# Optimization experiments

Measured on AMD Instinct MI355X. Metric: run time of the kernel, lower is better.

## Reference

```python
import jax, jax.numpy as jnp
import numpy as np

LEAK = 0.95
EPS = 1e-4
THRESH = 1.0


def spike_fn(x):
    # forward of SurrogateBPFunction: heaviside(x > 0)
    return (x > 0).astype(x.dtype)


def setup_inputs() -> dict:
    key = jax.random.key(0)
    k1, k2, k3 = jax.random.split(key, 3)
    T, B, D_in, H, C = 20, 512, 4096, 1024, 100
    z = jax.random.normal(k1, (T, B, D_in), dtype=jnp.float32)
    # xavier_uniform with gain=2: bound = 2 * sqrt(6/(fan_in+fan_out))
    b1 = 2.0 * np.sqrt(6.0 / (D_in + H))
    W1 = jax.random.uniform(k2, (H, D_in), dtype=jnp.float32, minval=-b1, maxval=b1)
    b2 = 2.0 * np.sqrt(6.0 / (H + C))
    W2 = jax.random.uniform(k3, (C, H), dtype=jnp.float32, minval=-b2, maxval=b2)
    bn_gamma = jnp.ones((T, H), dtype=jnp.float32)
    return {"z": z, "W1": W1, "bn_gamma": bn_gamma, "W2": W2}


def reference(z, W1, bn_gamma, W2):
    T = z.shape[0]
    B = z.shape[1]
    H = W1.shape[0]
    C = W2.shape[0]

    def step(carry, xs):
        mem1, mem2 = carry
        inp_t, gamma = xs  # inp_t: [B, D_in], gamma: [H]
        h = jnp.einsum('bd,hd->bh', inp_t, W1)  # fc1, no bias
        # BatchNorm1d (training-mode batch stats, affine weight, no bias)
        mean = h.mean(axis=0)
        var = h.var(axis=0)  # biased variance, matches torch BN
        h = gamma * (h - mean) * jax.lax.rsqrt(var + EPS)
        mem1 = LEAK * mem1 + h
        mem_thr = mem1 / THRESH - 1.0
        out = spike_fn(mem_thr)
        rst = jnp.where(mem_thr > 0, THRESH, 0.0).astype(mem1.dtype)
        mem1 = mem1 - rst
        mem2 = mem2 + jnp.einsum('bh,ch->bc', out, W2)
        return (mem1, mem2), None

    mem1_0 = jnp.zeros((B, H), dtype=z.dtype)
    mem2_0 = jnp.zeros((B, C), dtype=z.dtype)
    (mem1, mem2), _ = jax.lax.scan(step, (mem1_0, mem2_0), (z, bn_gamma))
    return mem2 / T
```

## Files before the change

### kernel.cpp

```cpp
#include <hip/hip_runtime.h>
#include <hip/hip_bf16.h>
#include <stdint.h>

typedef _Float16 half8 __attribute__((ext_vector_type(8)));
typedef float f32x4 __attribute__((ext_vector_type(4)));
typedef float f32x16 __attribute__((ext_vector_type(16)));

#define T_STEPS 20
#define B_SZ 512
#define D_IN 4096
#define H_SZ 1024
#define C_SZ 100
#define M_TOT (T_STEPS * B_SZ)
#define BK 32
#define KITERS (D_IN / BK)

__device__ __forceinline__ void gload16(const _Float16* g, _Float16* l) {
  __builtin_amdgcn_global_load_lds(
      (const __attribute__((address_space(1))) void*)g,
      (__attribute__((address_space(3))) void*)l, 16, 0, 0);
}

struct HL {
  half8 h;
  half8 l;
};
__device__ __forceinline__ HL split8(float4 a, float4 b) {
  HL r;
  auto p0 = __builtin_amdgcn_cvt_pkrtz(a.x, a.y);
  auto p1 = __builtin_amdgcn_cvt_pkrtz(a.z, a.w);
  auto p2 = __builtin_amdgcn_cvt_pkrtz(b.x, b.y);
  auto p3 = __builtin_amdgcn_cvt_pkrtz(b.z, b.w);
  r.h[0] = p0.x; r.h[1] = p0.y; r.h[2] = p1.x; r.h[3] = p1.y;
  r.h[4] = p2.x; r.h[5] = p2.y; r.h[6] = p3.x; r.h[7] = p3.y;
  auto q0 = __builtin_amdgcn_cvt_pkrtz(a.x - (float)p0.x, a.y - (float)p0.y);
  auto q1 = __builtin_amdgcn_cvt_pkrtz(a.z - (float)p1.x, a.w - (float)p1.y);
  auto q2 = __builtin_amdgcn_cvt_pkrtz(b.x - (float)p2.x, b.y - (float)p2.y);
  auto q3 = __builtin_amdgcn_cvt_pkrtz(b.z - (float)p3.x, b.w - (float)p3.y);
  r.l[0] = q0.x; r.l[1] = q0.y; r.l[2] = q1.x; r.l[3] = q1.y;
  r.l[4] = q2.x; r.l[5] = q2.y; r.l[6] = q3.x; r.l[7] = q3.y;
  return r;
}

__global__ __launch_bounds__(256) void k_prep_frag(
    const float* __restrict__ Z, _Float16* __restrict__ Azh,
    _Float16* __restrict__ Azl, const float* __restrict__ W1,
    _Float16* __restrict__ Wfh, _Float16* __restrict__ Wfl) {
  __shared__ float sL[32 * 256];

  const int cc = blockIdx.x;
  int rt = blockIdx.y >> 2;
  const int rb = blockIdx.y & 3;
  const float* src;
  _Float16 *dh, *dl;
  if (rt < 80) {
    src = Z; dh = Azh; dl = Azl;
  } else {
    rt -= 80; src = W1; dh = Wfh; dl = Wfl;
  }
  const int tid = threadIdx.x;
  const int lane64 = tid & 63;
  const int w4 = tid >> 6;

  const int row_base = rt * 128 + rb * 32;
  float4 v[8];
#pragma unroll
  for (int it = 0; it < 8; ++it) {
    const int row_local = it * 4 + w4;
    v[it] = *(const float4*)(src + (int64_t)(row_base + row_local) * D_IN +
                             cc * 256 + lane64 * 4);
  }
#pragma unroll
  for (int it = 0; it < 8; ++it) {
    const int row_local = it * 4 + w4;
    const int c = (lane64 * 4) ^ ((row_local & 7) << 2);
    *(float4*)&sL[row_local * 256 + c] = v[it];
  }
  __syncthreads();

  const int s = (tid >> 6) & 1;
  const int hi = (tid >> 5) & 1;
  const int l31 = tid & 31;
  const int q = s * 2 + hi;
  const int sw = (l31 & 7) << 2;
#pragma unroll
  for (int it2 = 0; it2 < 4; ++it2) {
    const int kil = it2 * 2 + (tid >> 7);
    const int c0 = kil * 32 + q * 8;
    float4 a = *(const float4*)&sL[l31 * 256 + (c0 ^ sw)];
    float4 b = *(const float4*)&sL[l31 * 256 + ((c0 + 4) ^ sw)];
    HL hl = split8(a, b);
    const int64_t d = ((int64_t)(rt * 128 + cc * 8 + kil)) * 4096 +
                      (rb * 128 + s * 64 + hi * 32 + l31) * 8;
    *(half8*)&dh[d] = hl.h;
    *(half8*)&dl[d] = hl.l;
  }
}

__global__ void k_prep_w2(const float* __restrict__ w2, _Float16* __restrict__ hi,
                          _Float16* __restrict__ lo) {
  int i = blockIdx.x * 256 + threadIdx.x;
  float v = (i < C_SZ * H_SZ) ? w2[i] : 0.0f;
  _Float16 h = (_Float16)v;
  hi[i] = h;
  lo[i] = (_Float16)(v - (float)h);
}

__global__ __launch_bounds__(256) void k_gemm1(
    const _Float16* __restrict__ Ahi, const _Float16* __restrict__ Alo,
    const _Float16* __restrict__ Whi, const _Float16* __restrict__ Wlo,
    float* __restrict__ Hbuf) {
  __shared__ _Float16 sAh[4096];
  __shared__ _Float16 sAl[4096];
  __shared__ _Float16 sWh[4096];
  __shared__ _Float16 sWl[4096];

  const int tid = threadIdx.x;
  const int lane = tid & 63;
  const int w = tid >> 6;

  const int bid = blockIdx.x;
  const int xcd = bid & 7;
  const int qb = bid >> 3;
  const int mt = xcd * 10 + (qb >> 3);
  const int nt = qb & 7;

  const int ls = w * 512 + lane * 8;
  const _Float16* gAh = Ahi + (int64_t)mt * (128 * 4096) + ls;
  const _Float16* gAl = Alo + (int64_t)mt * (128 * 4096) + ls;
  const _Float16* gWh = Whi + (int64_t)nt * (128 * 4096) + ls;
  const _Float16* gWl = Wlo + (int64_t)nt * (128 * 4096) + ls;

  const int wm = (w >> 1) * 64;
  const int wn = (w & 1) * 64;
  const int ra = (wm >> 4) * 512 + lane * 8;
  const int rbb = (wn >> 4) * 512 + lane * 8;

  f32x16 acc[2][2] = {};

  for (int ki = 0; ki < KITERS; ++ki) {
    const int64_t so = (int64_t)ki * 4096;
    __syncthreads();
    gload16(gAh + so, &sAh[ls]);
    gload16(gAh + so + 2048, &sAh[ls + 2048]);
    gload16(gAl + so, &sAl[ls]);
    gload16(gAl + so + 2048, &sAl[ls + 2048]);
    gload16(gWh + so, &sWh[ls]);
    gload16(gWh + so + 2048, &sWh[ls + 2048]);
    gload16(gWl + so, &sWl[ls]);
    gload16(gWl + so + 2048, &sWl[ls + 2048]);
    __syncthreads();

    half8 ah[2][2], al[2][2], bh[2][2], bl[2][2];
#pragma unroll
    for (int i = 0; i < 2; ++i) {
#pragma unroll
      for (int s = 0; s < 2; ++s) {
        ah[i][s] = *(const half8*)&sAh[ra + (i * 2 + s) * 512];
        al[i][s] = *(const half8*)&sAl[ra + (i * 2 + s) * 512];
        bh[i][s] = *(const half8*)&sWh[rbb + (i * 2 + s) * 512];
        bl[i][s] = *(const half8*)&sWl[rbb + (i * 2 + s) * 512];
      }
    }
#pragma unroll
    for (int a = 0; a < 2; ++a) {
#pragma unroll
      for (int b = 0; b < 2; ++b) {
#pragma unroll
        for (int s = 0; s < 2; ++s) {
          acc[a][b] = __builtin_amdgcn_mfma_f32_32x32x16_f16(ah[a][s], bh[b][s], acc[a][b], 0, 0, 0);
          acc[a][b] = __builtin_amdgcn_mfma_f32_32x32x16_f16(ah[a][s], bl[b][s], acc[a][b], 0, 0, 0);
          acc[a][b] = __builtin_amdgcn_mfma_f32_32x32x16_f16(al[a][s], bh[b][s], acc[a][b], 0, 0, 0);
        }
      }
    }
  }

  const int64_t m0 = (int64_t)mt * 128;
  const int n0 = nt * 128;
  const int l31 = lane & 31;
  const int h2 = lane >> 5;
#pragma unroll
  for (int a = 0; a < 2; ++a) {
#pragma unroll
    for (int b = 0; b < 2; ++b) {
      float* dst = Hbuf + (m0 + wm + a * 32 + h2 * 4) * H_SZ + n0 + wn + b * 32 + l31;
#pragma unroll
      for (int r4 = 0; r4 < 4; ++r4) {
#pragma unroll
        for (int r = 0; r < 4; ++r) {
          dst[(int64_t)(r4 * 8 + r) * H_SZ] = acc[a][b][r4 * 4 + r];
        }
      }
    }
  }
}

__global__ void k_stats(const float* __restrict__ Hbuf, const float* __restrict__ gamma,
                        float* __restrict__ scale, float* __restrict__ shift) {
  const int t = blockIdx.y;
  const int tx = threadIdx.x & 63;
  const int ty = threadIdx.x >> 6;
  const int h = blockIdx.x * 64 + tx;
  const float* p = Hbuf + ((int64_t)t * B_SZ + ty * 128) * H_SZ + h;
  float s = 0.f, s2 = 0.f;
#pragma unroll 8
  for (int i = 0; i < 128; ++i) {
    float v = p[(int64_t)i * H_SZ];
    s += v;
    s2 += v * v;
  }
  __shared__ float ss[4][64];
  __shared__ float sq[4][64];
  ss[ty][tx] = s;
  sq[ty][tx] = s2;
  __syncthreads();
  if (ty == 0) {
    float a = ss[0][tx] + ss[1][tx] + ss[2][tx] + ss[3][tx];
    float b = sq[0][tx] + sq[1][tx] + sq[2][tx] + sq[3][tx];
    const float mean = a * (1.0f / B_SZ);
    const float var = b * (1.0f / B_SZ) - mean * mean;
    const float rs = rsqrtf(var + 1e-4f);
    const float sc = gamma[t * H_SZ + h] * rs;
    scale[t * H_SZ + h] = sc;
    shift[t * H_SZ + h] = -mean * sc;
  }
}

__global__ void k_recur(const float* __restrict__ Hbuf, const float* __restrict__ scale,
                        const float* __restrict__ shift, _Float16* __restrict__ S) {
  const int idx = blockIdx.x * 256 + threadIdx.x;
  const int b = idx >> 10;
  const int h = idx & 1023;
  float mem = 0.f;
  int cnt = 0;
#pragma unroll
  for (int t = 0; t < T_STEPS; ++t) {
    float v = Hbuf[((int64_t)(t * B_SZ + b) << 10) + h];
    v = v * scale[(t << 10) + h] + shift[(t << 10) + h];
    mem = 0.95f * mem + v;
    if (mem - 1.0f > 0.0f) {
      ++cnt;
      mem -= 1.0f;
    }
  }
  S[idx] = (_Float16)cnt;
}

__global__ void k_gemm2(const _Float16* __restrict__ S, const _Float16* __restrict__ W2h,
                        const _Float16* __restrict__ W2l, float* __restrict__ out) {
  const int wid = threadIdx.x >> 6;
  const int lane = threadIdx.x & 63;
  const int m0 = blockIdx.y * 64 + wid * 16;
  const int n0 = blockIdx.x * 16;
  const int fr = lane & 15;
  const int quad = lane >> 4;

  const _Float16* sp = S + (int64_t)(m0 + fr) * H_SZ + quad * 8;
  const _Float16* wph = W2h + (int64_t)(n0 + fr) * H_SZ + quad * 8;
  const _Float16* wpl = W2l + (int64_t)(n0 + fr) * H_SZ + quad * 8;

  f32x4 acc = {0.f, 0.f, 0.f, 0.f};
#pragma unroll 4
  for (int k = 0; k < H_SZ; k += 32) {
    half8 a = *(const half8*)(sp + k);
    half8 bh = *(const half8*)(wph + k);
    half8 bl = *(const half8*)(wpl + k);
    acc = __builtin_amdgcn_mfma_f32_16x16x32_f16(a, bh, acc, 0, 0, 0);
    acc = __builtin_amdgcn_mfma_f32_16x16x32_f16(a, bl, acc, 0, 0, 0);
  }
  const int col = n0 + fr;
  if (col < C_SZ) {
#pragma unroll
    for (int r = 0; r < 4; ++r) {
      const int row = m0 + quad * 4 + r;
      out[row * C_SZ + col] = acc[r] * (1.0f / T_STEPS);
    }
  }
}

extern "C" void kernel_launch(void* const* d_in, const int* in_sizes, int n_in,
                              void* d_out, int out_size, void* d_ws, size_t ws_size,
                              hipStream_t stream) {
  const float* z = (const float*)d_in[0];
  const float* W1 = (const float*)d_in[1];
  const float* gamma = (const float*)d_in[2];
  const float* W2 = (const float*)d_in[3];
  float* out = (float*)d_out;

  char* ws = (char*)d_ws;
  size_t off = 0;
  auto alloc = [&](size_t bytes) -> void* {
    void* p = ws + off;
    off += (bytes + 255) & ~(size_t)255;
    return p;
  };
  _Float16* Azh = (_Float16*)alloc((size_t)M_TOT * D_IN * 2);
  _Float16* Azl = (_Float16*)alloc((size_t)M_TOT * D_IN * 2);
  _Float16* Wfh = (_Float16*)alloc((size_t)H_SZ * D_IN * 2);
  _Float16* Wfl = (_Float16*)alloc((size_t)H_SZ * D_IN * 2);
  float* Hbuf = (float*)alloc((size_t)M_TOT * H_SZ * 4);
  float* scale = (float*)alloc((size_t)T_STEPS * H_SZ * 4);
  float* shift = (float*)alloc((size_t)T_STEPS * H_SZ * 4);
  _Float16* S = (_Float16*)alloc((size_t)B_SZ * H_SZ * 2);
  _Float16* W2h = (_Float16*)alloc((size_t)112 * H_SZ * 2);
  _Float16* W2l = (_Float16*)alloc((size_t)112 * H_SZ * 2);

  dim3 gp(16, 352);
  k_prep_frag<<<gp, 256, 0, stream>>>(z, Azh, Azl, W1, Wfh, Wfl);
  k_prep_w2<<<(112 * H_SZ) / 256, 256, 0, stream>>>(W2, W2h, W2l);

  k_gemm1<<<640, 256, 0, stream>>>(Azh, Azl, Wfh, Wfl, Hbuf);

  dim3 gs(H_SZ / 64, T_STEPS);
  k_stats<<<gs, 256, 0, stream>>>(Hbuf, gamma, scale, shift);

  k_recur<<<(B_SZ * H_SZ) / 256, 256, 0, stream>>>(Hbuf, scale, shift, S);

  dim3 g2(7, 8);
  k_gemm2<<<g2, 256, 0, stream>>>(S, W2h, W2l, out);
}
```

Baseline: 556.2 us.

## Double-buffer LDS tiles in fc1 GEMM to overlap loads with MFMA

Splits each shared-memory operand buffer into two stages and restructures the K loop so the next tile's global-to-LDS loads are issued before computing on the current tile. This is meant to hide global load latency behind MFMA work and drop one barrier per iteration. It doubles LDS usage per block, which may lower occupancy.

```diff
diff --git a/kernel.cpp b/kernel.cpp
--- a/kernel.cpp
+++ b/kernel.cpp
@@ -110,10 +110,10 @@
     const _Float16* __restrict__ Ahi, const _Float16* __restrict__ Alo,
     const _Float16* __restrict__ Whi, const _Float16* __restrict__ Wlo,
     float* __restrict__ Hbuf) {
-  __shared__ _Float16 sAh[4096];
-  __shared__ _Float16 sAl[4096];
-  __shared__ _Float16 sWh[4096];
-  __shared__ _Float16 sWl[4096];
+  __shared__ _Float16 sAh[2][4096];
+  __shared__ _Float16 sAl[2][4096];
+  __shared__ _Float16 sWh[2][4096];
+  __shared__ _Float16 sWl[2][4096];
 
   const int tid = threadIdx.x;
   const int lane = tid & 63;
@@ -138,28 +138,28 @@
 
   f32x16 acc[2][2] = {};
 
-  for (int ki = 0; ki < KITERS; ++ki) {
+  auto stage = [&](int buf, int ki) {
     const int64_t so = (int64_t)ki * 4096;
-    __syncthreads();
-    gload16(gAh + so, &sAh[ls]);
-    gload16(gAh + so + 2048, &sAh[ls + 2048]);
-    gload16(gAl + so, &sAl[ls]);
-    gload16(gAl + so + 2048, &sAl[ls + 2048]);
-    gload16(gWh + so, &sWh[ls]);
-    gload16(gWh + so + 2048, &sWh[ls + 2048]);
-    gload16(gWl + so, &sWl[ls]);
-    gload16(gWl + so + 2048, &sWl[ls + 2048]);
-    __syncthreads();
-
+    gload16(gAh + so, &sAh[buf][ls]);
+    gload16(gAh + so + 2048, &sAh[buf][ls + 2048]);
+    gload16(gAl + so, &sAl[buf][ls]);
+    gload16(gAl + so + 2048, &sAl[buf][ls + 2048]);
+    gload16(gWh + so, &sWh[buf][ls]);
+    gload16(gWh + so + 2048, &sWh[buf][ls + 2048]);
+    gload16(gWl + so, &sWl[buf][ls]);
+    gload16(gWl + so + 2048, &sWl[buf][ls + 2048]);
+  };
+
+  auto compute = [&](int buf) {
     half8 ah[2][2], al[2][2], bh[2][2], bl[2][2];
 #pragma unroll
     for (int i = 0; i < 2; ++i) {
 #pragma unroll
       for (int s = 0; s < 2; ++s) {
-        ah[i][s] = *(const half8*)&sAh[ra + (i * 2 + s) * 512];
-        al[i][s] = *(const half8*)&sAl[ra + (i * 2 + s) * 512];
-        bh[i][s] = *(const half8*)&sWh[rbb + (i * 2 + s) * 512];
-        bl[i][s] = *(const half8*)&sWl[rbb + (i * 2 + s) * 512];
+        ah[i][s] = *(const half8*)&sAh[buf][ra + (i * 2 + s) * 512];
+        al[i][s] = *(const half8*)&sAl[buf][ra + (i * 2 + s) * 512];
+        bh[i][s] = *(const half8*)&sWh[buf][rbb + (i * 2 + s) * 512];
+        bl[i][s] = *(const half8*)&sWl[buf][rbb + (i * 2 + s) * 512];
       }
     }
 #pragma unroll
@@ -174,6 +174,18 @@
         }
       }
     }
+  };
+
+  stage(0, 0);
+  __syncthreads();
+
+  for (int ki = 0; ki < KITERS; ki += 2) {
+    if (ki + 1 < KITERS) stage(1, ki + 1);
+    compute(0);
+    __syncthreads();
+    if (ki + 2 < KITERS) stage(0, ki + 2);
+    compute(1);
+    __syncthreads();
   }
 
   const int64_t m0 = (int64_t)mt * 128;
```

Measured after the change: 706.3 us. +27.0%, slower.

## Split gemm1 K dimension in two with partial planes summed downstream

Applied to the files above, without the earlier changes.

Splits the first GEMM's K loop into two halves, doubling the block count, and writes each half's result to a separate partial-sum plane. The stats and recurrence kernels read both planes and add them. This is meant to improve CU utilization and wave balance for the large GEMM. In exchange it doubles the workspace and the global traffic for the hidden activations.

```diff
diff --git a/kernel.cpp b/kernel.cpp
--- a/kernel.cpp
+++ b/kernel.cpp
@@ -14,6 +14,8 @@
 #define M_TOT (T_STEPS * B_SZ)
 #define BK 32
 #define KITERS (D_IN / BK)
+#define KHALF (KITERS / 2)
+#define HPLANE ((int64_t)M_TOT * H_SZ)
 
 __device__ __forceinline__ void gload16(const _Float16* g, _Float16* l) {
   __builtin_amdgcn_global_load_lds(
@@ -109,7 +111,7 @@
 __global__ __launch_bounds__(256) void k_gemm1(
     const _Float16* __restrict__ Ahi, const _Float16* __restrict__ Alo,
     const _Float16* __restrict__ Whi, const _Float16* __restrict__ Wlo,
-    float* __restrict__ Hbuf) {
+    float* __restrict__ Hpart) {
   __shared__ _Float16 sAh[4096];
   __shared__ _Float16 sAl[4096];
   __shared__ _Float16 sWh[4096];
@@ -121,9 +123,12 @@
 
   const int bid = blockIdx.x;
   const int xcd = bid & 7;
-  const int qb = bid >> 3;
-  const int mt = xcd * 10 + (qb >> 3);
-  const int nt = qb & 7;
+  const int q = bid >> 3;
+  const int mtl = q >> 4;
+  const int r = q & 15;
+  const int nt = r >> 1;
+  const int kh = r & 1;
+  const int mt = xcd * 10 + mtl;
 
   const int ls = w * 512 + lane * 8;
   const _Float16* gAh = Ahi + (int64_t)mt * (128 * 4096) + ls;
@@ -138,7 +143,8 @@
 
   f32x16 acc[2][2] = {};
 
-  for (int ki = 0; ki < KITERS; ++ki) {
+  const int k0 = kh * KHALF;
+  for (int ki = k0; ki < k0 + KHALF; ++ki) {
     const int64_t so = (int64_t)ki * 4096;
     __syncthreads();
     gload16(gAh + so, &sAh[ls]);
@@ -176,6 +182,7 @@
     }
   }
 
+  float* Hb = Hpart + (int64_t)kh * HPLANE;
   const int64_t m0 = (int64_t)mt * 128;
   const int n0 = nt * 128;
   const int l31 = lane & 31;
@@ -184,29 +191,30 @@
   for (int a = 0; a < 2; ++a) {
 #pragma unroll
     for (int b = 0; b < 2; ++b) {
-      float* dst = Hbuf + (m0 + wm + a * 32 + h2 * 4) * H_SZ + n0 + wn + b * 32 + l31;
+      float* dst = Hb + (m0 + wm + a * 32 + h2 * 4) * H_SZ + n0 + wn + b * 32 + l31;
 #pragma unroll
       for (int r4 = 0; r4 < 4; ++r4) {
 #pragma unroll
-        for (int r = 0; r < 4; ++r) {
-          dst[(int64_t)(r4 * 8 + r) * H_SZ] = acc[a][b][r4 * 4 + r];
+        for (int rr = 0; rr < 4; ++rr) {
+          dst[(int64_t)(r4 * 8 + rr) * H_SZ] = acc[a][b][r4 * 4 + rr];
         }
       }
     }
   }
 }
 
-__global__ void k_stats(const float* __restrict__ Hbuf, const float* __restrict__ gamma,
+__global__ void k_stats(const float* __restrict__ Hpart, const float* __restrict__ gamma,
                         float* __restrict__ scale, float* __restrict__ shift) {
   const int t = blockIdx.y;
   const int tx = threadIdx.x & 63;
   const int ty = threadIdx.x >> 6;
   const int h = blockIdx.x * 64 + tx;
-  const float* p = Hbuf + ((int64_t)t * B_SZ + ty * 128) * H_SZ + h;
+  const float* p0 = Hpart + ((int64_t)t * B_SZ + ty * 128) * H_SZ + h;
+  const float* p1 = p0 + HPLANE;
   float s = 0.f, s2 = 0.f;
 #pragma unroll 8
   for (int i = 0; i < 128; ++i) {
-    float v = p[(int64_t)i * H_SZ];
+    float v = p0[(int64_t)i * H_SZ] + p1[(int64_t)i * H_SZ];
     s += v;
     s2 += v * v;
   }
@@ -227,7 +235,7 @@
   }
 }
 
-__global__ void k_recur(const float* __restrict__ Hbuf, const float* __restrict__ scale,
+__global__ void k_recur(const float* __restrict__ Hpart, const float* __restrict__ scale,
                         const float* __restrict__ shift, _Float16* __restrict__ S) {
   const int idx = blockIdx.x * 256 + threadIdx.x;
   const int b = idx >> 10;
@@ -236,7 +244,8 @@
   int cnt = 0;
 #pragma unroll
   for (int t = 0; t < T_STEPS; ++t) {
-    float v = Hbuf[((int64_t)(t * B_SZ + b) << 10) + h];
+    const int64_t i = ((int64_t)(t * B_SZ + b) << 10) + h;
+    float v = Hpart[i] + Hpart[i + HPLANE];
     v = v * scale[(t << 10) + h] + shift[(t << 10) + h];
     mem = 0.95f * mem + v;
     if (mem - 1.0f > 0.0f) {
@@ -299,7 +308,7 @@
   _Float16* Azl = (_Float16*)alloc((size_t)M_TOT * D_IN * 2);
   _Float16* Wfh = (_Float16*)alloc((size_t)H_SZ * D_IN * 2);
   _Float16* Wfl = (_Float16*)alloc((size_t)H_SZ * D_IN * 2);
-  float* Hbuf = (float*)alloc((size_t)M_TOT * H_SZ * 4);
+  float* Hpart = (float*)alloc((size_t)2 * M_TOT * H_SZ * 4);
   float* scale = (float*)alloc((size_t)T_STEPS * H_SZ * 4);
   float* shift = (float*)alloc((size_t)T_STEPS * H_SZ * 4);
   _Float16* S = (_Float16*)alloc((size_t)B_SZ * H_SZ * 2);
@@ -310,12 +319,12 @@
   k_prep_frag<<<gp, 256, 0, stream>>>(z, Azh, Azl, W1, Wfh, Wfl);
   k_prep_w2<<<(112 * H_SZ) / 256, 256, 0, stream>>>(W2, W2h, W2l);
 
-  k_gemm1<<<640, 256, 0, stream>>>(Azh, Azl, Wfh, Wfl, Hbuf);
+  k_gemm1<<<1280, 256, 0, stream>>>(Azh, Azl, Wfh, Wfl, Hpart);
 
   dim3 gs(H_SZ / 64, T_STEPS);
-  k_stats<<<gs, 256, 0, stream>>>(Hbuf, gamma, scale, shift);
-
-  k_recur<<<(B_SZ * H_SZ) / 256, 256, 0, stream>>>(Hbuf, scale, shift, S);
+  k_stats<<<gs, 256, 0, stream>>>(Hpart, gamma, scale, shift);
+
+  k_recur<<<(B_SZ * H_SZ) / 256, 256, 0, stream>>>(Hpart, scale, shift, S);
 
   dim3 g2(7, 8);
   k_gemm2<<<g2, 256, 0, stream>>>(S, W2h, W2l, out);
```

Measured after the change: 541.9 us. 2.6% less time.
